# Kernel tuning notes

Hardware: AMD Instinct MI355X
Metric: run time of the kernel (lower is better)

The kernel has to match this reference:

```python
import jax, jax.numpy as jnp
import numpy as np

T, B, I, H = 2048, 64, 256, 512

def setup_inputs() -> dict:
    key = jax.random.key(0)
    ks = jax.random.split(key, 9)
    s = 1.0 / np.sqrt(I + H)  # torch Linear default init scale
    return {
        "x": jax.random.normal(ks[0], (T, B, I), dtype=jnp.float32),
        "Wf": jax.random.uniform(ks[1], (H, I + H), jnp.float32, -s, s),
        "bf": jax.random.uniform(ks[2], (H,), jnp.float32, -s, s),
        "Wi": jax.random.uniform(ks[3], (H, I + H), jnp.float32, -s, s),
        "bi": jax.random.uniform(ks[4], (H,), jnp.float32, -s, s),
        "Wc": jax.random.uniform(ks[5], (H, I + H), jnp.float32, -s, s),
        "bc": jax.random.uniform(ks[6], (H,), jnp.float32, -s, s),
        "Wo": jax.random.uniform(ks[7], (H, I + H), jnp.float32, -s, s),
        "bo": jax.random.uniform(ks[8], (H,), jnp.float32, -s, s),
    }

def reference(x, Wf, bf, Wi, bi, Wc, bc, Wo, bo):
    # x: [T, B, I]; initial h, mem are zeros as in the torch module
    Bsz = x.shape[1]
    h0 = jnp.zeros((Bsz, H), dtype=x.dtype)
    c0 = jnp.zeros((Bsz, H), dtype=x.dtype)

    def step(carry, xt):
        h, c = carry
        hx = jnp.concatenate([h, xt], axis=1)  # cat order (h, xt), [B, H+I]
        f = jax.nn.sigmoid(hx @ Wf.T + bf)
        i = jax.nn.sigmoid(hx @ Wi.T + bi)
        c_new = f * c + i * jnp.tanh(hx @ Wc.T + bc)
        o = jax.nn.sigmoid(hx @ Wo.T + bo)
        h_new = o * jnp.tanh(c_new)
        return (h_new, c_new), h_new

    (h_last, c_last), output = jax.lax.scan(step, (h0, c0), x)
    return output, h_last, c_last
```

## Files before the change

kernel.cpp:

```cpp
#include <hip/hip_runtime.h>
#include <hip/hip_bf16.h>


#define T_STEPS 2048
#define BATCH   64
#define IN_F    256
#define HID     512
#define KTOT    768
#define BHSZ    (BATCH*HID)
#define NBLK    128

typedef __attribute__((ext_vector_type(8))) short  short8;
typedef __attribute__((ext_vector_type(4))) float  f32x4;

__device__ __forceinline__ f32x4 mfma16(short8 a, short8 b, f32x4 c) {
    return __builtin_amdgcn_mfma_f32_16x16x32_bf16(a, b, c, 0, 0, 0);
}
__device__ __forceinline__ short bf16bits(float f) {
    return (short)__builtin_bit_cast(unsigned short, __float2bfloat16(f));
}
__device__ __forceinline__ short8 cvt8(const float* __restrict__ p) {
    f32x4 a = *(const f32x4*)p;
    f32x4 b = *(const f32x4*)(p + 4);
    short8 r;
    r[0] = bf16bits(a[0]); r[1] = bf16bits(a[1]); r[2] = bf16bits(a[2]); r[3] = bf16bits(a[3]);
    r[4] = bf16bits(b[0]); r[5] = bf16bits(b[1]); r[6] = bf16bits(b[2]); r[7] = bf16bits(b[3]);
    return r;
}
__device__ __forceinline__ float sigf(float x)      { return 1.f / (1.f + __expf(-x)); }
__device__ __forceinline__ float tanh_fast(float x) { return 2.f / (1.f + __expf(-2.f * x)) - 1.f; }

__global__ void __launch_bounds__(128, 1)
lstm_persistent(const float* __restrict__ x,
                const float* __restrict__ Wf, const float* __restrict__ bfv,
                const float* __restrict__ Wi, const float* __restrict__ biv,
                const float* __restrict__ Wc, const float* __restrict__ bcv,
                const float* __restrict__ Wo, const float* __restrict__ bov,
                float* __restrict__ out, unsigned* cnt, short* hping)
{
    const int tid  = threadIdx.x;
    const int wv   = tid >> 6;
    const int lane = tid & 63;
    const int bn   = lane & 15;
    const int quad = lane >> 4;
    const int mg   = blockIdx.x & 3;
    const int ng   = blockIdx.x >> 2;
    const int hbase = ng << 4;
    const int m0    = mg << 4;

    short8 Ba[24], Bb[24];
    {
        const float* ra = (wv ? Wc : Wf) + (size_t)(hbase + bn) * KTOT + quad * 8;
        const float* rb = (wv ? Wo : Wi) + (size_t)(hbase + bn) * KTOT + quad * 8;
        #pragma unroll
        for (int kt = 0; kt < 24; ++kt) {
            Ba[kt] = cvt8(ra + kt * 32);
            Bb[kt] = cvt8(rb + kt * 32);
        }
    }

    const int ec = tid & 15;
    const int er = tid >> 4;
    const float vbf = bfv[hbase + ec];
    const float vbi = biv[hbase + ec];
    const float vbc = bcv[hbase + ec];
    const float vbo = bov[hbase + ec];
    float c0 = 0.f, c1 = 0.f;

    __shared__ float glds[4][16][17];

    #pragma unroll 1
    for (int t = 0; t < T_STEPS; ++t) {
        f32x4 aA = {0.f,0.f,0.f,0.f}, aA2 = aA, aB = aA, aB2 = aA;

        {
            const float* xr = x + ((size_t)t * BATCH + m0 + bn) * IN_F + quad * 8;
            #pragma unroll
            for (int kt = 0; kt < 8; ++kt) {
                short8 av = cvt8(xr + kt * 32);
                if (kt & 1) { aA2 = mfma16(av, Ba[16 + kt], aA2); aB2 = mfma16(av, Bb[16 + kt], aB2); }
                else        { aA  = mfma16(av, Ba[16 + kt], aA ); aB  = mfma16(av, Bb[16 + kt], aB ); }
            }
        }

        if (t > 0) {
            if (tid == 0) {
                const unsigned tgt = (unsigned)NBLK * (unsigned)t;
                while (__hip_atomic_load(cnt, __ATOMIC_RELAXED, __HIP_MEMORY_SCOPE_AGENT) < tgt)
                    __builtin_amdgcn_s_sleep(1);
                __builtin_amdgcn_fence(__ATOMIC_ACQUIRE, "agent");
            }
            __syncthreads();
            const short* hr = hping + (size_t)((t - 1) & 1) * BHSZ + (m0 + bn) * HID + quad * 8;
            #pragma unroll
            for (int kt = 0; kt < 16; ++kt) {
                short8 av = *(const short8*)(hr + kt * 32);
                if (kt & 1) { aA2 = mfma16(av, Ba[kt], aA2); aB2 = mfma16(av, Bb[kt], aB2); }
                else        { aA  = mfma16(av, Ba[kt], aA ); aB  = mfma16(av, Bb[kt], aB ); }
            }
        }
        aA += aA2; aB += aB2;

        #pragma unroll
        for (int r = 0; r < 4; ++r) {
            glds[wv * 2 + 0][quad * 4 + r][bn] = aA[r];
            glds[wv * 2 + 1][quad * 4 + r][bn] = aB[r];
        }
        __syncthreads();

        const float f0 = sigf(glds[0][er][ec] + vbf);
        const float i0 = sigf(glds[1][er][ec] + vbi);
        const float g0 = tanh_fast(glds[2][er][ec] + vbc);
        const float o0 = sigf(glds[3][er][ec] + vbo);
        c0 = f0 * c0 + i0 * g0;
        const float h0 = o0 * tanh_fast(c0);

        const float f1 = sigf(glds[0][er + 8][ec] + vbf);
        const float i1 = sigf(glds[1][er + 8][ec] + vbi);
        const float g1 = tanh_fast(glds[2][er + 8][ec] + vbc);
        const float o1 = sigf(glds[3][er + 8][ec] + vbo);
        c1 = f1 * c1 + i1 * g1;
        const float h1 = o1 * tanh_fast(c1);

        const size_t ob = (size_t)t * BHSZ + (size_t)(m0 + er) * HID + hbase + ec;
        out[ob]           = h0;
        out[ob + 8 * HID] = h1;
        short* hw = hping + (size_t)(t & 1) * BHSZ + (size_t)(m0 + er) * HID + hbase + ec;
        hw[0]       = bf16bits(h0);
        hw[8 * HID] = bf16bits(h1);
        if (t == T_STEPS - 1) {
            const size_t ol = (size_t)T_STEPS * BHSZ + (size_t)(m0 + er) * HID + hbase + ec;
            out[ol]           = h0;
            out[ol + 8 * HID] = h1;
        }

        __syncthreads();
        if (tid == 0)
            __hip_atomic_fetch_add(cnt, 1u, __ATOMIC_RELEASE, __HIP_MEMORY_SCOPE_AGENT);
    }

    const size_t oc = (size_t)T_STEPS * BHSZ + BHSZ + (size_t)(m0 + er) * HID + hbase + ec;
    out[oc]           = c0;
    out[oc + 8 * HID] = c1;
}

extern "C" void kernel_launch(void* const* d_in, const int* in_sizes, int n_in,
                              void* d_out, int out_size, void* d_ws, size_t ws_size,
                              hipStream_t stream) {
    hipMemsetAsync(d_ws, 0, 256, stream);
    unsigned* cnt  = (unsigned*)d_ws;
    short*   hping = (short*)((char*)d_ws + 1024);
    lstm_persistent<<<NBLK, 128, 0, stream>>>(
        (const float*)d_in[0],
        (const float*)d_in[1], (const float*)d_in[2],
        (const float*)d_in[3], (const float*)d_in[4],
        (const float*)d_in[5], (const float*)d_in[6],
        (const float*)d_in[7], (const float*)d_in[8],
        (float*)d_out, cnt, hping);
}
```

Baseline: 18.71 ms.

## Shrink grid to 32 blocks with per-block step flags instead of shared counter

```diff
diff --git a/kernel.cpp b/kernel.cpp
--- a/kernel.cpp
+++ b/kernel.cpp
@@ -8,10 +8,13 @@
 #define HID     512
 #define KTOT    768
 #define BHSZ    (BATCH*HID)
-#define NBLK    128
+#define NBLK    32
+#define NTHR    256
+#define FSTR    32
 
 typedef __attribute__((ext_vector_type(8))) short  short8;
 typedef __attribute__((ext_vector_type(4))) float  f32x4;
+typedef __attribute__((ext_vector_type(2))) float  f32x2;
 
 __device__ __forceinline__ f32x4 mfma16(short8 a, short8 b, f32x4 c) {
     return __builtin_amdgcn_mfma_f32_16x16x32_bf16(a, b, c, 0, 0, 0);
@@ -30,131 +33,184 @@
 __device__ __forceinline__ float sigf(float x)      { return 1.f / (1.f + __expf(-x)); }
 __device__ __forceinline__ float tanh_fast(float x) { return 2.f / (1.f + __expf(-2.f * x)) - 1.f; }
 
-__global__ void __launch_bounds__(128, 1)
+__global__ void __launch_bounds__(NTHR, 1)
 lstm_persistent(const float* __restrict__ x,
                 const float* __restrict__ Wf, const float* __restrict__ bfv,
                 const float* __restrict__ Wi, const float* __restrict__ biv,
                 const float* __restrict__ Wc, const float* __restrict__ bcv,
                 const float* __restrict__ Wo, const float* __restrict__ bov,
-                float* __restrict__ out, unsigned* cnt, short* hping)
+                float* __restrict__ out, unsigned* flags, short* hping)
 {
     const int tid  = threadIdx.x;
-    const int wv   = tid >> 6;
+    const int w    = tid >> 6;
+    const int gp   = w & 1;
+    const int mp   = w >> 1;
+    const int m0   = mp << 5;
     const int lane = tid & 63;
     const int bn   = lane & 15;
     const int quad = lane >> 4;
-    const int mg   = blockIdx.x & 3;
-    const int ng   = blockIdx.x >> 2;
+    const int ng   = blockIdx.x;
     const int hbase = ng << 4;
-    const int m0    = mg << 4;
-
-    short8 Ba[24], Bb[24];
+
+    __shared__ short8 wx[2][2][8][64];
+    __shared__ float  glds[4][64][17];
+
+    const float* Wa = gp ? Wc : Wf;
+    const float* Wb = gp ? Wo : Wi;
+    short8 Ba[16], Bb[16];
     {
-        const float* ra = (wv ? Wc : Wf) + (size_t)(hbase + bn) * KTOT + quad * 8;
-        const float* rb = (wv ? Wo : Wi) + (size_t)(hbase + bn) * KTOT + quad * 8;
+        const float* ra = Wa + (size_t)(hbase + bn) * KTOT + quad * 8;
+        const float* rb = Wb + (size_t)(hbase + bn) * KTOT + quad * 8;
         #pragma unroll
-        for (int kt = 0; kt < 24; ++kt) {
+        for (int kt = 0; kt < 16; ++kt) {
             Ba[kt] = cvt8(ra + kt * 32);
             Bb[kt] = cvt8(rb + kt * 32);
         }
+        if (mp == 0) {
+            #pragma unroll
+            for (int kt = 0; kt < 8; ++kt) {
+                wx[gp][0][kt][lane] = cvt8(ra + 512 + kt * 32);
+                wx[gp][1][kt][lane] = cvt8(rb + 512 + kt * 32);
+            }
+        }
     }
 
-    const int ec = tid & 15;
-    const int er = tid >> 4;
-    const float vbf = bfv[hbase + ec];
-    const float vbi = biv[hbase + ec];
-    const float vbc = bcv[hbase + ec];
-    const float vbo = bov[hbase + ec];
-    float c0 = 0.f, c1 = 0.f;
-
-    __shared__ float glds[4][16][17];
+    const int er = tid >> 3;
+    const int ec = (tid & 7) << 1;
+    const f32x2 vbf = *(const f32x2*)(bfv + hbase + ec);
+    const f32x2 vbi = *(const f32x2*)(biv + hbase + ec);
+    const f32x2 vbc = *(const f32x2*)(bcv + hbase + ec);
+    const f32x2 vbo = *(const f32x2*)(bov + hbase + ec);
+    float c00 = 0.f, c01 = 0.f, c10 = 0.f, c11 = 0.f;
+
+    __syncthreads();
 
     #pragma unroll 1
     for (int t = 0; t < T_STEPS; ++t) {
-        f32x4 aA = {0.f,0.f,0.f,0.f}, aA2 = aA, aB = aA, aB2 = aA;
-
-        {
-            const float* xr = x + ((size_t)t * BATCH + m0 + bn) * IN_F + quad * 8;
+        f32x4 z = {0.f, 0.f, 0.f, 0.f};
+        f32x4 aA0 = z, aA0b = z, aB0 = z, aB0b = z;
+        f32x4 aA1 = z, aA1b = z, aB1 = z, aB1b = z;
+
+        {
+            const float* xr0 = x + ((size_t)t * BATCH + m0 + bn) * IN_F + quad * 8;
+            const float* xr1 = xr0 + 16 * IN_F;
             #pragma unroll
             for (int kt = 0; kt < 8; ++kt) {
-                short8 av = cvt8(xr + kt * 32);
-                if (kt & 1) { aA2 = mfma16(av, Ba[16 + kt], aA2); aB2 = mfma16(av, Bb[16 + kt], aB2); }
-                else        { aA  = mfma16(av, Ba[16 + kt], aA ); aB  = mfma16(av, Bb[16 + kt], aB ); }
+                short8 wa = wx[gp][0][kt][lane];
+                short8 wb = wx[gp][1][kt][lane];
+                short8 a0 = cvt8(xr0 + kt * 32);
+                short8 a1 = cvt8(xr1 + kt * 32);
+                if (kt & 1) { aA0b = mfma16(a0, wa, aA0b); aB0b = mfma16(a0, wb, aB0b);
+                              aA1b = mfma16(a1, wa, aA1b); aB1b = mfma16(a1, wb, aB1b); }
+                else        { aA0  = mfma16(a0, wa, aA0 ); aB0  = mfma16(a0, wb, aB0 );
+                              aA1  = mfma16(a1, wa, aA1 ); aB1  = mfma16(a1, wb, aB1 ); }
             }
         }
 
         if (t > 0) {
-            if (tid == 0) {
-                const unsigned tgt = (unsigned)NBLK * (unsigned)t;
-                while (__hip_atomic_load(cnt, __ATOMIC_RELAXED, __HIP_MEMORY_SCOPE_AGENT) < tgt)
+            if (tid < 64) {
+                const unsigned tgt = (unsigned)t;
+                const unsigned* fp = flags + (size_t)(tid & 31) * FSTR;
+                while (__hip_atomic_load(fp, __ATOMIC_RELAXED, __HIP_MEMORY_SCOPE_AGENT) < tgt)
                     __builtin_amdgcn_s_sleep(1);
                 __builtin_amdgcn_fence(__ATOMIC_ACQUIRE, "agent");
             }
             __syncthreads();
-            const short* hr = hping + (size_t)((t - 1) & 1) * BHSZ + (m0 + bn) * HID + quad * 8;
+            const short* hr0 = hping + (size_t)((t - 1) & 1) * BHSZ + (size_t)(m0 + bn) * HID + quad * 8;
+            const short* hr1 = hr0 + 16 * HID;
             #pragma unroll
             for (int kt = 0; kt < 16; ++kt) {
-                short8 av = *(const short8*)(hr + kt * 32);
-                if (kt & 1) { aA2 = mfma16(av, Ba[kt], aA2); aB2 = mfma16(av, Bb[kt], aB2); }
-                else        { aA  = mfma16(av, Ba[kt], aA ); aB  = mfma16(av, Bb[kt], aB ); }
-            }
-        }
-        aA += aA2; aB += aB2;
-
-        #pragma unroll
-        for (int r = 0; r < 4; ++r) {
-            glds[wv * 2 + 0][quad * 4 + r][bn] = aA[r];
-            glds[wv * 2 + 1][quad * 4 + r][bn] = aB[r];
+                short8 a0 = *(const short8*)(hr0 + kt * 32);
+                short8 a1 = *(const short8*)(hr1 + kt * 32);
+                if (kt & 1) { aA0b = mfma16(a0, Ba[kt], aA0b); aB0b = mfma16(a0, Bb[kt], aB0b);
+                              aA1b = mfma16(a1, Ba[kt], aA1b); aB1b = mfma16(a1, Bb[kt], aB1b); }
+                else        { aA0  = mfma16(a0, Ba[kt], aA0 ); aB0  = mfma16(a0, Bb[kt], aB0 );
+                              aA1  = mfma16(a1, Ba[kt], aA1 ); aB1  = mfma16(a1, Bb[kt], aB1 ); }
+            }
+        }
+        aA0 += aA0b; aB0 += aB0b; aA1 += aA1b; aB1 += aB1b;
+
+        {
+            const int wr = m0 + quad * 4;
+            #pragma unroll
+            for (int r = 0; r < 4; ++r) {
+                glds[gp * 2 + 0][wr + r][bn]      = aA0[r];
+                glds[gp * 2 + 1][wr + r][bn]      = aB0[r];
+                glds[gp * 2 + 0][wr + 16 + r][bn] = aA1[r];
+                glds[gp * 2 + 1][wr + 16 + r][bn] = aB1[r];
+            }
         }
         __syncthreads();
 
-        const float f0 = sigf(glds[0][er][ec] + vbf);
-        const float i0 = sigf(glds[1][er][ec] + vbi);
-        const float g0 = tanh_fast(glds[2][er][ec] + vbc);
-        const float o0 = sigf(glds[3][er][ec] + vbo);
-        c0 = f0 * c0 + i0 * g0;
-        const float h0 = o0 * tanh_fast(c0);
-
-        const float f1 = sigf(glds[0][er + 8][ec] + vbf);
-        const float i1 = sigf(glds[1][er + 8][ec] + vbi);
-        const float g1 = tanh_fast(glds[2][er + 8][ec] + vbc);
-        const float o1 = sigf(glds[3][er + 8][ec] + vbo);
-        c1 = f1 * c1 + i1 * g1;
-        const float h1 = o1 * tanh_fast(c1);
-
-        const size_t ob = (size_t)t * BHSZ + (size_t)(m0 + er) * HID + hbase + ec;
-        out[ob]           = h0;
-        out[ob + 8 * HID] = h1;
-        short* hw = hping + (size_t)(t & 1) * BHSZ + (size_t)(m0 + er) * HID + hbase + ec;
-        hw[0]       = bf16bits(h0);
-        hw[8 * HID] = bf16bits(h1);
-        if (t == T_STEPS - 1) {
-            const size_t ol = (size_t)T_STEPS * BHSZ + (size_t)(m0 + er) * HID + hbase + ec;
-            out[ol]           = h0;
-            out[ol + 8 * HID] = h1;
+        const float f0 = sigf(glds[0][er][ec]      + vbf.x);
+        const float f1 = sigf(glds[0][er][ec + 1]  + vbf.y);
+        const float i0 = sigf(glds[1][er][ec]      + vbi.x);
+        const float i1 = sigf(glds[1][er][ec + 1]  + vbi.y);
+        const float g0 = tanh_fast(glds[2][er][ec]     + vbc.x);
+        const float g1 = tanh_fast(glds[2][er][ec + 1] + vbc.y);
+        const float o0 = sigf(glds[3][er][ec]      + vbo.x);
+        const float o1 = sigf(glds[3][er][ec + 1]  + vbo.y);
+        c00 = f0 * c00 + i0 * g0;  const float h00 = o0 * tanh_fast(c00);
+        c01 = f1 * c01 + i1 * g1;  const float h01 = o1 * tanh_fast(c01);
+
+        const float F0 = sigf(glds[0][er + 32][ec]      + vbf.x);
+        const float F1 = sigf(glds[0][er + 32][ec + 1]  + vbf.y);
+        const float I0 = sigf(glds[1][er + 32][ec]      + vbi.x);
+        const float I1 = sigf(glds[1][er + 32][ec + 1]  + vbi.y);
+        const float G0 = tanh_fast(glds[2][er + 32][ec]     + vbc.x);
+        const float G1 = tanh_fast(glds[2][er + 32][ec + 1] + vbc.y);
+        const float O0 = sigf(glds[3][er + 32][ec]      + vbo.x);
+        const float O1 = sigf(glds[3][er + 32][ec + 1]  + vbo.y);
+        c10 = F0 * c10 + I0 * G0;  const float h10 = O0 * tanh_fast(c10);
+        c11 = F1 * c11 + I1 * G1;  const float h11 = O1 * tanh_fast(c11);
+
+        {
+            short* hw = hping + (size_t)(t & 1) * BHSZ + (size_t)er * HID + hbase + ec;
+            const unsigned hp0 = (unsigned)(unsigned short)bf16bits(h00)
+                               | ((unsigned)(unsigned short)bf16bits(h01) << 16);
+            const unsigned hp1 = (unsigned)(unsigned short)bf16bits(h10)
+                               | ((unsigned)(unsigned short)bf16bits(h11) << 16);
+            __builtin_nontemporal_store(hp0, (unsigned*)hw);
+            __builtin_nontemporal_store(hp1, (unsigned*)(hw + 32 * HID));
         }
 
         __syncthreads();
         if (tid == 0)
-            __hip_atomic_fetch_add(cnt, 1u, __ATOMIC_RELEASE, __HIP_MEMORY_SCOPE_AGENT);
+            __hip_atomic_store(flags + (size_t)blockIdx.x * FSTR, (unsigned)(t + 1),
+                               __ATOMIC_RELEASE, __HIP_MEMORY_SCOPE_AGENT);
+
+        {
+            const size_t ob = (size_t)t * BHSZ + (size_t)er * HID + hbase + ec;
+            f32x2 v0 = {h00, h01}, v1 = {h10, h11};
+            __builtin_nontemporal_store(v0, (f32x2*)(out + ob));
+            __builtin_nontemporal_store(v1, (f32x2*)(out + ob + 32 * HID));
+            if (t == T_STEPS - 1) {
+                const size_t ol = (size_t)T_STEPS * BHSZ + (size_t)er * HID + hbase + ec;
+                __builtin_nontemporal_store(v0, (f32x2*)(out + ol));
+                __builtin_nontemporal_store(v1, (f32x2*)(out + ol + 32 * HID));
+            }
+        }
     }
 
-    const size_t oc = (size_t)T_STEPS * BHSZ + BHSZ + (size_t)(m0 + er) * HID + hbase + ec;
-    out[oc]           = c0;
-    out[oc + 8 * HID] = c1;
+    {
+        const size_t oc = (size_t)T_STEPS * BHSZ + BHSZ + (size_t)er * HID + hbase + ec;
+        f32x2 v0 = {c00, c01}, v1 = {c10, c11};
+        __builtin_nontemporal_store(v0, (f32x2*)(out + oc));
+        __builtin_nontemporal_store(v1, (f32x2*)(out + oc + 32 * HID));
+    }
 }
 
 extern "C" void kernel_launch(void* const* d_in, const int* in_sizes, int n_in,
                               void* d_out, int out_size, void* d_ws, size_t ws_size,
                               hipStream_t stream) {
-    hipMemsetAsync(d_ws, 0, 256, stream);
-    unsigned* cnt  = (unsigned*)d_ws;
-    short*   hping = (short*)((char*)d_ws + 1024);
-    lstm_persistent<<<NBLK, 128, 0, stream>>>(
+    hipMemsetAsync(d_ws, 0, 4096, stream);
+    unsigned* flags = (unsigned*)d_ws;
+    short*    hping = (short*)((char*)d_ws + 4096);
+    lstm_persistent<<<NBLK, NTHR, 0, stream>>>(
         (const float*)d_in[0],
         (const float*)d_in[1], (const float*)d_in[2],
         (const float*)d_in[3], (const float*)d_in[4],
         (const float*)d_in[5], (const float*)d_in[6],
         (const float*)d_in[7], (const float*)d_in[8],
-        (float*)d_out, cnt, hping);
-}
+        (float*)d_out, flags, hping);
+}
```

Result: slower. 35.54 ms (+90.0%).
